# Performance work log

Measured on AMD Instinct MI355X. Metric: run time of the kernel, lower is better.

Reference implementation:

```python
import jax, jax.numpy as jnp
import numpy as np


def _oneplus(x):
    return 1.0 + jax.nn.softplus(x)


def _content(mem, keys, beta):
    # mem: [B,A,M], keys: [B,K,M], beta: [B,K] -> weights [B,K,A]
    eps = 1e-6
    dot = jnp.einsum('bam,bkm->bka', mem, keys)
    mn = jnp.linalg.norm(mem, axis=-1)   # [B,A]
    kn = jnp.linalg.norm(keys, axis=-1)  # [B,K]
    cos = dot / (kn[:, :, None] * mn[:, None, :] + eps)
    return jax.nn.softmax(beta[:, :, None] * cos, axis=-1)


def setup_inputs():
    key = jax.random.key(0)
    ks = jax.random.split(key, 20)
    B, I, H, O, A, M, R = 16, 256, 512, 256, 1024, 64, 4
    IF = R * M + R + M + 1 + M + M + R + 2 + 3 * R  # 471
    def lin(k, fi, fo):
        return jax.random.normal(k, (fi, fo)) / np.sqrt(fi)
    eye = jnp.eye(A)
    return dict(
        x=jax.random.normal(ks[0], (B, I)),
        h_prev=jax.random.normal(ks[1], (B, H)) * 0.1,
        c_prev=jax.random.normal(ks[2], (B, H)) * 0.1,
        mem_prev=jax.random.normal(ks[3], (B, A, M)) * 0.1,
        rw_prev=jax.nn.softmax(jax.random.normal(ks[4], (B, R, A)), axis=-1),
        ww_prev=jax.nn.softmax(jax.random.normal(ks[5], (B, A)), axis=-1),
        usage_prev=jax.random.uniform(ks[6], (B, A)),
        prec_prev=jax.nn.softmax(jax.random.normal(ks[7], (B, A)), axis=-1),
        link_prev=jax.random.uniform(ks[8], (B, A, A)) * 1e-3 * (1.0 - eye),
        rv_prev=jax.random.normal(ks[9], (B, R * M)) * 0.1,
        Wx=lin(ks[10], I + R * M, 4 * H),
        Wh=lin(ks[11], H, 4 * H),
        b_lstm=jnp.zeros((4 * H,)),
        W_hid=lin(ks[12], H, O),
        b_hid=jnp.zeros((O,)),
        W_if=lin(ks[13], H, IF),
        b_if=jnp.zeros((IF,)),
        W_rd=lin(ks[14], R * M, O),
        b_rd=jnp.zeros((O,)),
    )


def reference(x, h_prev, c_prev, mem_prev, rw_prev, ww_prev, usage_prev, prec_prev,
              link_prev, rv_prev, Wx, Wh, b_lstm, W_hid, b_hid, W_if, b_if, W_rd, b_rd):
    B, R, A = rw_prev.shape
    M = mem_prev.shape[-1]
    # --- controller LSTM over [input, prev read vectors] ---
    z = jnp.concatenate([x, rv_prev], axis=-1) @ Wx + h_prev @ Wh + b_lstm
    i, f, g, o = jnp.split(z, 4, axis=-1)
    c = jax.nn.sigmoid(f) * c_prev + jax.nn.sigmoid(i) * jnp.tanh(g)
    h = jax.nn.sigmoid(o) * jnp.tanh(c)
    out_hidden = h @ W_hid + b_hid
    iface = h @ W_if + b_if
    # --- split interface vector ---
    p = 0
    k_r = iface[:, p:p + R * M].reshape(B, R, M); p += R * M
    beta_r = _oneplus(iface[:, p:p + R]); p += R
    k_w = iface[:, p:p + M]; p += M
    beta_w = _oneplus(iface[:, p:p + 1]); p += 1
    erase = jax.nn.sigmoid(iface[:, p:p + M]); p += M
    write_v = iface[:, p:p + M]; p += M
    free = jax.nn.sigmoid(iface[:, p:p + R]); p += R
    g_a = jax.nn.sigmoid(iface[:, p:p + 1]); p += 1
    g_w = jax.nn.sigmoid(iface[:, p:p + 1]); p += 1
    pi = jax.nn.softmax(iface[:, p:p + 3 * R].reshape(B, R, 3), axis=-1)
    # --- usage / retention ---
    psi = jnp.prod(1.0 - free[:, :, None] * rw_prev, axis=1)  # [B,A]
    usage = (usage_prev + ww_prev - usage_prev * ww_prev) * psi
    # --- allocation weighting via sorted usage ---
    idx = jnp.argsort(usage, axis=-1)
    su = jnp.take_along_axis(usage, idx, axis=-1)
    cp = jnp.cumprod(su, axis=-1)
    cp_excl = jnp.concatenate([jnp.ones_like(cp[:, :1]), cp[:, :-1]], axis=-1)
    a_sorted = (1.0 - su) * cp_excl
    alloc = jnp.take_along_axis(a_sorted, jnp.argsort(idx, axis=-1), axis=-1)
    # --- write weighting + memory edit ---
    c_w = _content(mem_prev, k_w[:, None, :], beta_w)[:, 0]  # [B,A]
    ww = g_w * (g_a * alloc + (1.0 - g_a) * c_w)
    mem = mem_prev * (1.0 - ww[:, :, None] * erase[:, None, :]) + ww[:, :, None] * write_v[:, None, :]
    # --- temporal link / precedence ---
    link = (1.0 - ww[:, :, None] - ww[:, None, :]) * link_prev + ww[:, :, None] * prec_prev[:, None, :]
    link = link * (1.0 - jnp.eye(A, dtype=link.dtype))
    prec = (1.0 - jnp.sum(ww, axis=-1, keepdims=True)) * prec_prev + ww
    # --- read weighting: backward / content / forward modes ---
    fwd_w = jnp.einsum('bij,brj->bri', link, rw_prev)
    bwd_w = jnp.einsum('bji,brj->bri', link, rw_prev)
    c_r = _content(mem, k_r, beta_r)
    w_r = pi[..., 0:1] * bwd_w + pi[..., 1:2] * c_r + pi[..., 2:3] * fwd_w
    rv = jnp.einsum('bra,bam->brm', w_r, mem).reshape(B, R * M)
    return out_hidden + rv @ W_rd + b_rd
```

## Files before the change

kernel.cpp:

```cpp
#include <hip/hip_runtime.h>
#include <math.h>


__device__ __forceinline__ float sigf(float x){ return 1.0f/(1.0f+expf(-x)); }
__device__ __forceinline__ float softplusf(float x){ return fmaxf(x,0.0f)+log1pf(expf(-fabsf(x))); }

__global__ __launch_bounds__(256) void k_lstm_part(const float* __restrict__ x,
    const float* __restrict__ rv, const float* __restrict__ hp,
    const float* __restrict__ Wx, const float* __restrict__ Wh,
    float* __restrict__ zpart){
  __shared__ float inp[8][64];
  int ct = blockIdx.x, kt = blockIdx.y, bg = blockIdx.z, t = threadIdx.x;
  for (int i = t; i < 512; i += 256){
    int bb = i >> 6, kk = i & 63;
    int k = kt*64 + kk, b = bg*8 + bb;
    float v = (k < 256) ? x[b*256+k] : (k < 512) ? rv[b*256 + k-256] : hp[b*512 + k-512];
    inp[bb][kk] = v;
  }
  __syncthreads();
  int col = ct*256 + t;
  float acc[8];
  #pragma unroll
  for (int bb = 0; bb < 8; ++bb) acc[bb] = 0.0f;
  for (int kk = 0; kk < 64; ++kk){
    int k = kt*64 + kk;
    float w = (k < 512) ? Wx[(long)k*2048 + col] : Wh[(long)(k-512)*2048 + col];
    #pragma unroll
    for (int bb = 0; bb < 8; ++bb) acc[bb] += inp[bb][kk]*w;
  }
  #pragma unroll
  for (int bb = 0; bb < 8; ++bb)
    zpart[((long)kt*16 + bg*8 + bb)*2048 + col] = acc[bb];
}

__global__ void k_lstm_fin(const float* __restrict__ zpart, const float* __restrict__ bl,
                           const float* __restrict__ cp, float* __restrict__ h_ws){
  int jt = blockIdx.x, b = blockIdx.y, j = jt*128 + threadIdx.x;
  float zi = bl[j], zf = bl[512+j], zg = bl[1024+j], zo = bl[1536+j];
  for (int kt = 0; kt < 16; ++kt){
    const float* zp = zpart + ((long)kt*16 + b)*2048;
    zi += zp[j]; zf += zp[512+j]; zg += zp[1024+j]; zo += zp[1536+j];
  }
  float c = sigf(zf)*cp[b*512+j] + sigf(zi)*tanhf(zg);
  h_ws[b*512+j] = sigf(zo)*tanhf(c);
}

__global__ __launch_bounds__(256) void k_iface_part(const float* __restrict__ h_ws,
    const float* __restrict__ W_if, const float* __restrict__ W_hid,
    float* __restrict__ ifpart){
  __shared__ float hh[8][32];
  int ct = blockIdx.x, kt = blockIdx.y, bg = blockIdx.z, t = threadIdx.x;
  {
    int bb = t >> 5, kk = t & 31;
    hh[bb][kk] = h_ws[(bg*8 + bb)*512 + kt*32 + kk];
  }
  __syncthreads();
  int col = ct*256 + t;
  float acc[8];
  #pragma unroll
  for (int bb = 0; bb < 8; ++bb) acc[bb] = 0.0f;
  if (col < 727){
    for (int kk = 0; kk < 32; ++kk){
      int k = kt*32 + kk;
      float w = (col < 471) ? W_if[(long)k*471 + col] : W_hid[(long)k*256 + (col-471)];
      #pragma unroll
      for (int bb = 0; bb < 8; ++bb) acc[bb] += hh[bb][kk]*w;
    }
    #pragma unroll
    for (int bb = 0; bb < 8; ++bb)
      ifpart[((long)kt*16 + bg*8 + bb)*768 + col] = acc[bb];
  }
}

__global__ void k_iface_fin(const float* __restrict__ ifpart, const float* __restrict__ b_if,
                            const float* __restrict__ b_hid, float* __restrict__ ifr_ws,
                            float* __restrict__ outh_ws){
  int b = blockIdx.x, t = threadIdx.x;
  if (t >= 727) return;
  float s = (t < 471) ? b_if[t] : b_hid[t-471];
  for (int kt = 0; kt < 16; ++kt) s += ifpart[((long)kt*16 + b)*768 + t];
  if (t < 471) ifr_ws[b*512 + t] = s;
  else         outh_ws[b*256 + (t-471)] = s;
}

__global__ void k_act_alloc(const float* __restrict__ ifr_ws, const float* __restrict__ rw_prev,
                            const float* __restrict__ ww_prev, const float* __restrict__ usage_prev,
                            float* __restrict__ ifa_ws, float* __restrict__ alloc_ws){
  __shared__ float sifa[480];
  __shared__ unsigned long long keys[1024];
  __shared__ float cpp[1024];
  int b = blockIdx.x, t = threadIdx.x;
  const float* ifr = ifr_ws + b*512;
  if (t < 471){
    float v = ifr[t], o = v;
    if ((t >= 256 && t < 260) || t == 324) o = 1.0f + softplusf(v);
    else if ((t >= 325 && t < 389) || (t >= 453 && t < 459)) o = sigf(v);
    sifa[t] = o;
  }
  __syncthreads();
  if (t < 4){
    float p0 = ifr[459+t*3+0], p1 = ifr[459+t*3+1], p2 = ifr[459+t*3+2];
    float mx = fmaxf(p0, fmaxf(p1,p2));
    float e0 = expf(p0-mx), e1 = expf(p1-mx), e2 = expf(p2-mx);
    float s = e0+e1+e2;
    sifa[459+t*3+0]=e0/s; sifa[459+t*3+1]=e1/s; sifa[459+t*3+2]=e2/s;
  }
  __syncthreads();
  if (t < 471) ifa_ws[b*512 + t] = sifa[t];
  float f0 = sifa[453], f1 = sifa[454], f2 = sifa[455], f3 = sifa[456];
  float psi = (1.f - f0*rw_prev[(long)(b*4+0)*1024 + t])
            * (1.f - f1*rw_prev[(long)(b*4+1)*1024 + t])
            * (1.f - f2*rw_prev[(long)(b*4+2)*1024 + t])
            * (1.f - f3*rw_prev[(long)(b*4+3)*1024 + t]);
  float uu = usage_prev[b*1024+t], w = ww_prev[b*1024+t];
  float uval = (uu + w - uu*w) * psi;
  unsigned int ub = __float_as_uint(uval);
  unsigned int k32 = ub ^ (((int)ub >> 31) | 0x80000000u);
  keys[t] = ((unsigned long long)k32 << 32) | (unsigned int)t;
  __syncthreads();
  for (int k = 2; k <= 1024; k <<= 1){
    for (int j = k >> 1; j > 0; j >>= 1){
      int ixj = t ^ j;
      if (ixj > t){
        unsigned long long a = keys[t], c = keys[ixj];
        bool up = ((t & k) == 0);
        if ((a > c) == up){ keys[t] = c; keys[ixj] = a; }
      }
      __syncthreads();
    }
  }
  unsigned long long key = keys[t];
  unsigned int hk = (unsigned int)(key >> 32);
  unsigned int ob = (hk & 0x80000000u) ? (hk ^ 0x80000000u) : ~hk;
  float su = __uint_as_float(ob);
  int oi = (int)(key & 1023u);
  cpp[t] = su;
  __syncthreads();
  for (int off = 1; off < 1024; off <<= 1){
    float tmp = (t >= off) ? cpp[t-off] : 1.0f;
    __syncthreads();
    cpp[t] *= tmp;
    __syncthreads();
  }
  float cpe = (t == 0) ? 1.0f : cpp[t-1];
  alloc_ws[b*1024 + oi] = (1.0f - su) * cpe;
}

__global__ __launch_bounds__(256) void k_wscore(const float* __restrict__ mem_prev,
    const float* __restrict__ ifa_ws, float* __restrict__ wsc_ws){
  int at = blockIdx.x, b = blockIdx.y;
  int t = threadIdx.x, w = t >> 6, m = t & 63;
  const float* ifa = ifa_ws + b*512;
  float kwm = ifa[260+m], beta = ifa[324];
  float knsq = kwm*kwm;
  for (int o = 32; o > 0; o >>= 1) knsq += __shfl_xor(knsq, o);
  float kn = sqrtf(knsq);
  for (int rr = 0; rr < 16; ++rr){
    int a = at*64 + w*16 + rr;
    float v = mem_prev[((long)b*1024+a)*64+m];
    float d = v*kwm, sq = v*v;
    for (int o = 32; o > 0; o >>= 1){ d += __shfl_xor(d,o); sq += __shfl_xor(sq,o); }
    if (m == 0) wsc_ws[b*1024+a] = beta*d/(kn*sqrtf(sq)+1e-6f);
  }
}

__global__ void k_cw_ww(const float* __restrict__ wsc_ws, const float* __restrict__ ifa_ws,
                        const float* __restrict__ alloc_ws, const float* __restrict__ rw_prev,
                        float* __restrict__ ww_ws, float* __restrict__ e_ws){
  __shared__ float red[1024];
  int b = blockIdx.x, t = threadIdx.x;
  const float* ifa = ifa_ws + b*512;
  float g_a = ifa[457], g_w = ifa[458];
  float sc = wsc_ws[b*1024+t];
  red[t] = sc; __syncthreads();
  for (int s = 512; s > 0; s >>= 1){ if (t < s) red[t] = fmaxf(red[t], red[t+s]); __syncthreads(); }
  float mx = red[0]; __syncthreads();
  float e = expf(sc - mx);
  red[t] = e; __syncthreads();
  for (int s = 512; s > 0; s >>= 1){ if (t < s) red[t] += red[t+s]; __syncthreads(); }
  float cw = e / red[0];
  float ww = g_w*(g_a*alloc_ws[b*1024+t] + (1.0f-g_a)*cw);
  ww_ws[b*1024+t] = ww;
  #pragma unroll
  for (int r = 0; r < 4; ++r)
    e_ws[(long)(b*4+r)*1024 + t] = ww * rw_prev[(long)(b*4+r)*1024 + t];
}

__global__ __launch_bounds__(256) void k_score(const float* __restrict__ mem_prev,
    const float* __restrict__ ww_ws, const float* __restrict__ ifa_ws,
    float* __restrict__ mnorm_ws, float* __restrict__ rdot_ws){
  int at = blockIdx.x, b = blockIdx.y;
  int t = threadIdx.x, w = t >> 6, m = t & 63;
  const float* ifa = ifa_ws + b*512;
  float er = ifa[325+m], wv = ifa[389+m];
  float k0 = ifa[m], k1 = ifa[64+m], k2 = ifa[128+m], k3 = ifa[192+m];
  for (int rr = 0; rr < 16; ++rr){
    int a = at*64 + w*16 + rr;
    float ww = ww_ws[b*1024+a];
    float v = mem_prev[((long)b*1024+a)*64+m]*(1.0f - ww*er) + ww*wv;
    float sq = v*v, d0 = v*k0, d1 = v*k1, d2 = v*k2, d3 = v*k3;
    for (int o = 32; o > 0; o >>= 1){
      sq += __shfl_xor(sq,o); d0 += __shfl_xor(d0,o); d1 += __shfl_xor(d1,o);
      d2 += __shfl_xor(d2,o); d3 += __shfl_xor(d3,o);
    }
    if (m == 0){
      mnorm_ws[b*1024+a] = sqrtf(sq);
      rdot_ws[(long)(b*4+0)*1024+a] = d0; rdot_ws[(long)(b*4+1)*1024+a] = d1;
      rdot_ws[(long)(b*4+2)*1024+a] = d2; rdot_ws[(long)(b*4+3)*1024+a] = d3;
    }
  }
}

__global__ __launch_bounds__(256) void k_linkfb(const float* __restrict__ link_prev,
    const float* __restrict__ rw_prev, const float* __restrict__ e_ws,
    const float* __restrict__ prec_prev, const float* __restrict__ ww_ws,
    float* __restrict__ fwd_part, float* __restrict__ bwd_part){
  __shared__ float Lt[64][68];
  int band = blockIdx.x, ct = blockIdx.y, b = blockIdx.z, t = threadIdx.x;
  int r = t >> 6, lane = t & 63;
  int ru = __builtin_amdgcn_readfirstlane(r);
  const float4* L4 = (const float4*)link_prev;
  #pragma unroll
  for (int q = 0; q < 4; ++q){
    int idx = t + 256*q;
    int row = idx >> 4, c4 = idx & 15;
    float4 v = L4[((long)b << 18) + (long)(band*64+row)*256 + ct*16 + c4];
    *(float4*)&Lt[row][c4*4] = v;
  }
  const float* aJ = rw_prev + (long)(b*4+ru)*1024 + ct*64;
  const float* eJ = e_ws    + (long)(b*4+ru)*1024 + ct*64;
  const float* aI = rw_prev + (long)(b*4+ru)*1024 + band*64;
  const float* eI = e_ws    + (long)(b*4+ru)*1024 + band*64;
  float pv = prec_prev[b*1024 + ct*64 + lane] * aJ[lane];
  float wvs = eI[lane];
  for (int o = 32; o > 0; o >>= 1){ pv += __shfl_xor(pv,o); wvs += __shfl_xor(wvs,o); }
  float wwi = ww_ws[b*1024 + band*64 + lane];
  float wwc = ww_ws[b*1024 + ct*64 + lane];
  float pc  = prec_prev[b*1024 + ct*64 + lane];
  __syncthreads();
  float A1 = 0.0f, A2 = 0.0f;
  for (int jc = 0; jc < 64; jc += 4){
    float4 Lv = *(const float4*)&Lt[lane][jc];
    A1 += Lv.x*aJ[jc] + Lv.y*aJ[jc+1] + Lv.z*aJ[jc+2] + Lv.w*aJ[jc+3];
    A2 += Lv.x*eJ[jc] + Lv.y*eJ[jc+1] + Lv.z*eJ[jc+2] + Lv.w*eJ[jc+3];
  }
  float facc = (1.0f - wwi)*A1 - A2 + wwi*pv;
  float B1 = 0.0f, B2 = 0.0f;
  for (int rowl = 0; rowl < 64; ++rowl){
    float Lv = Lt[rowl][lane];
    B1 += Lv * aI[rowl];
    B2 += Lv * eI[rowl];
  }
  float bacc = (1.0f - wwc)*B1 - B2 + pc*wvs;
  if (band == ct){
    float D = ((1.0f - 2.0f*wwi)*Lt[lane][lane] + wwi*pc)*aJ[lane];
    facc -= D;
    bacc -= D;
  }
  fwd_part[(long)ct*65536 + (long)(b*4+r)*1024 + band*64 + lane] = facc;
  bwd_part[(long)band*65536 + (long)(b*4+r)*1024 + ct*64 + lane] = bacc;
}

__global__ void k_fbred(const float* __restrict__ fwd_part, const float* __restrict__ bwd_part,
                        float* __restrict__ fwd_ws, float* __restrict__ bwd_ws){
  int idx = blockIdx.x*1024 + threadIdx.x;
  float f = 0.0f, bsum = 0.0f;
  #pragma unroll
  for (int c = 0; c < 16; ++c){
    f    += fwd_part[(long)c*65536 + idx];
    bsum += bwd_part[(long)c*65536 + idx];
  }
  fwd_ws[idx] = f;
  bwd_ws[idx] = bsum;
}

__global__ void k_read(const float* __restrict__ rdot_ws, const float* __restrict__ mnorm_ws,
                       const float* __restrict__ ifa_ws, const float* __restrict__ fwd_ws,
                       const float* __restrict__ bwd_ws, const float* __restrict__ mem_prev,
                       const float* __restrict__ ww_ws, float* __restrict__ rv_ws){
  __shared__ float red[1024]; __shared__ float wrs[1024]; __shared__ float wwsh[1024];
  __shared__ float par[1];
  int r = blockIdx.x, b = blockIdx.y, t = threadIdx.x;
  const float* ifa = ifa_ws + b*512;
  if (t == 0){
    float s = 0;
    for (int m = 0; m < 64; ++m){ float v = ifa[r*64+m]; s += v*v; }
    par[0] = sqrtf(s);
  }
  wwsh[t] = ww_ws[b*1024+t];
  __syncthreads();
  float kn = par[0], beta = ifa[256 + r];
  float sc = beta * rdot_ws[(long)(b*4+r)*1024 + t] / (kn*mnorm_ws[b*1024+t] + 1e-6f);
  red[t] = sc; __syncthreads();
  for (int s = 512; s > 0; s >>= 1){ if (t < s) red[t] = fmaxf(red[t], red[t+s]); __syncthreads(); }
  float mx = red[0]; __syncthreads();
  float e = expf(sc - mx);
  red[t] = e; __syncthreads();
  for (int s = 512; s > 0; s >>= 1){ if (t < s) red[t] += red[t+s]; __syncthreads(); }
  float cr = e / red[0];
  __syncthreads();
  float p0 = ifa[459+3*r], p1 = ifa[460+3*r], p2 = ifa[461+3*r];
  wrs[t] = p0*bwd_ws[(long)(b*4+r)*1024 + t] + p1*cr + p2*fwd_ws[(long)(b*4+r)*1024 + t];
  __syncthreads();
  int m = t & 63, ch = t >> 6;
  float er = ifa[325+m], wv = ifa[389+m];
  float acc = 0;
  for (int q = 0; q < 64; ++q){
    int a = ch*64 + q;
    float w = wwsh[a];
    float v = mem_prev[((long)b*1024 + a)*64 + m]*(1.0f - w*er) + w*wv;
    acc += wrs[a]*v;
  }
  red[ch*64 + m] = acc;
  __syncthreads();
  if (t < 64){
    float s = 0;
    for (int c2 = 0; c2 < 16; ++c2) s += red[c2*64 + t];
    rv_ws[(b*4+r)*64 + t] = s;
  }
}

__global__ void k_out(const float* __restrict__ outh_ws, const float* __restrict__ rv_ws,
                      const float* __restrict__ W_rd, const float* __restrict__ b_rd,
                      float* __restrict__ out){
  __shared__ float rvs[256]; __shared__ float part[4][256];
  int b = blockIdx.x, t = threadIdx.x;
  int o = t & 255, kq = t >> 8;
  if (t < 256) rvs[t] = rv_ws[b*256 + t];
  __syncthreads();
  float acc = 0.0f;
  for (int q = kq*64; q < kq*64 + 64; ++q) acc += rvs[q]*W_rd[(long)q*256 + o];
  part[kq][o] = acc;
  __syncthreads();
  if (t < 256)
    out[b*256+t] = outh_ws[b*256+t] + b_rd[t] + part[0][t] + part[1][t] + part[2][t] + part[3][t];
}

extern "C" void kernel_launch(void* const* d_in, const int* in_sizes, int n_in,
                              void* d_out, int out_size, void* d_ws, size_t ws_size,
                              hipStream_t stream){
  const float* x          = (const float*)d_in[0];
  const float* h_prev     = (const float*)d_in[1];
  const float* c_prev     = (const float*)d_in[2];
  const float* mem_prev   = (const float*)d_in[3];
  const float* rw_prev    = (const float*)d_in[4];
  const float* ww_prev    = (const float*)d_in[5];
  const float* usage_prev = (const float*)d_in[6];
  const float* prec_prev  = (const float*)d_in[7];
  const float* link_prev  = (const float*)d_in[8];
  const float* rv_prev    = (const float*)d_in[9];
  const float* Wx         = (const float*)d_in[10];
  const float* Wh         = (const float*)d_in[11];
  const float* b_lstm     = (const float*)d_in[12];
  const float* W_hid      = (const float*)d_in[13];
  const float* b_hid      = (const float*)d_in[14];
  const float* W_if       = (const float*)d_in[15];
  const float* b_if       = (const float*)d_in[16];
  const float* W_rd       = (const float*)d_in[17];
  const float* b_rd       = (const float*)d_in[18];
  float* out = (float*)d_out;

  float* ws = (float*)d_ws;
  float* h_ws     = ws + 0;
  float* ifr_ws   = ws + 8192;
  float* ifa_ws   = ws + 16384;
  float* outh_ws  = ws + 24576;
  float* alloc_ws = ws + 28672;
  float* ww_ws    = ws + 45056;
  float* mnorm_ws = ws + 61440;
  float* wsc_ws   = ws + 77824;
  float* rv_ws    = ws + 94208;
  float* fwd_ws   = ws + 98304;
  float* bwd_ws   = ws + 163840;
  float* rdot_ws  = ws + 229376;
  float* e_ws     = ws + 294912;
  float* zpart    = ws + 360448;
  float* ifpart   = ws + 884736;
  float* fwd_part = ws + 1081344;
  float* bwd_part = ws + 2129920;

  k_lstm_part<<<dim3(8,16,2),256,0,stream>>>(x, rv_prev, h_prev, Wx, Wh, zpart);
  k_lstm_fin<<<dim3(4,16),128,0,stream>>>(zpart, b_lstm, c_prev, h_ws);
  k_iface_part<<<dim3(3,16,2),256,0,stream>>>(h_ws, W_if, W_hid, ifpart);
  k_iface_fin<<<16,768,0,stream>>>(ifpart, b_if, b_hid, ifr_ws, outh_ws);
  k_act_alloc<<<16,1024,0,stream>>>(ifr_ws, rw_prev, ww_prev, usage_prev, ifa_ws, alloc_ws);
  k_wscore<<<dim3(16,16),256,0,stream>>>(mem_prev, ifa_ws, wsc_ws);
  k_cw_ww<<<16,1024,0,stream>>>(wsc_ws, ifa_ws, alloc_ws, rw_prev, ww_ws, e_ws);
  k_score<<<dim3(16,16),256,0,stream>>>(mem_prev, ww_ws, ifa_ws, mnorm_ws, rdot_ws);
  k_linkfb<<<dim3(16,16,16),256,0,stream>>>(link_prev, rw_prev, e_ws, prec_prev, ww_ws,
                                            fwd_part, bwd_part);
  k_fbred<<<64,1024,0,stream>>>(fwd_part, bwd_part, fwd_ws, bwd_ws);
  k_read<<<dim3(4,16),1024,0,stream>>>(rdot_ws, mnorm_ws, ifa_ws, fwd_ws, bwd_ws,
                                       mem_prev, ww_ws, rv_ws);
  k_out<<<16,1024,0,stream>>>(outh_ws, rv_ws, W_rd, b_rd, out);
}
```

Baseline: 240.2 us.

## Use wave shuffles for sort, scan and softmax; fuse partial reduction into read

Bitonic sort stages with stride under 64 now exchange keys through wavefront shuffles instead of shared memory and barriers. The cumulative-product scan becomes a per-wave shuffle scan followed by a cross-wave prefix, and the softmax reductions in the write and read kernels become wave reductions plus a 16-entry combine. The separate forward/backward partial-sum kernel is removed and its 16-way sum folded into the read kernel, saving a launch and a round trip through global memory. The score kernels also move to 512-thread blocks with fewer rows per wave, which changes the per-thread work split.

```diff
diff --git a/kernel.cpp b/kernel.cpp
--- a/kernel.cpp
+++ b/kernel.cpp
@@ -88,8 +88,9 @@
                             float* __restrict__ ifa_ws, float* __restrict__ alloc_ws){
   __shared__ float sifa[480];
   __shared__ unsigned long long keys[1024];
-  __shared__ float cpp[1024];
+  __shared__ float wtot[16];
   int b = blockIdx.x, t = threadIdx.x;
+  int lane = t & 63, wid = t >> 6;
   const float* ifr = ifr_ws + b*512;
   if (t < 471){
     float v = ifr[t], o = v;
@@ -116,37 +117,44 @@
   float uval = (uu + w - uu*w) * psi;
   unsigned int ub = __float_as_uint(uval);
   unsigned int k32 = ub ^ (((int)ub >> 31) | 0x80000000u);
-  keys[t] = ((unsigned long long)k32 << 32) | (unsigned int)t;
-  __syncthreads();
-  for (int k = 2; k <= 1024; k <<= 1){
-    for (int j = k >> 1; j > 0; j >>= 1){
-      int ixj = t ^ j;
-      if (ixj > t){
-        unsigned long long a = keys[t], c = keys[ixj];
-        bool up = ((t & k) == 0);
-        if ((a > c) == up){ keys[t] = c; keys[ixj] = a; }
+  unsigned long long key = ((unsigned long long)k32 << 32) | (unsigned int)t;
+  for (int kk2 = 2; kk2 <= 1024; kk2 <<= 1){
+    for (int j = kk2 >> 1; j > 0; j >>= 1){
+      unsigned long long other;
+      if (j >= 64){
+        keys[t] = key;
+        __syncthreads();
+        other = keys[t ^ j];
+        __syncthreads();
+      } else {
+        other = __shfl_xor(key, j);
       }
-      __syncthreads();
+      bool up = ((t & kk2) == 0);
+      bool keepMin = (((t & j) == 0) == up);
+      if (keepMin ? (other < key) : (other > key)) key = other;
     }
   }
-  unsigned long long key = keys[t];
   unsigned int hk = (unsigned int)(key >> 32);
   unsigned int ob = (hk & 0x80000000u) ? (hk ^ 0x80000000u) : ~hk;
   float su = __uint_as_float(ob);
   int oi = (int)(key & 1023u);
-  cpp[t] = su;
-  __syncthreads();
-  for (int off = 1; off < 1024; off <<= 1){
-    float tmp = (t >= off) ? cpp[t-off] : 1.0f;
-    __syncthreads();
-    cpp[t] *= tmp;
-    __syncthreads();
-  }
-  float cpe = (t == 0) ? 1.0f : cpp[t-1];
+  float s = su;
+  #pragma unroll
+  for (int off = 1; off < 64; off <<= 1){
+    float v = __shfl_up(s, off);
+    if (lane >= off) s *= v;
+  }
+  if (lane == 63) wtot[wid] = s;
+  __syncthreads();
+  float wpre = 1.0f;
+  for (int w2 = 0; w2 < wid; ++w2) wpre *= wtot[w2];
+  float ex = __shfl_up(s, 1);
+  if (lane == 0) ex = 1.0f;
+  float cpe = ex * wpre;
   alloc_ws[b*1024 + oi] = (1.0f - su) * cpe;
 }
 
-__global__ __launch_bounds__(256) void k_wscore(const float* __restrict__ mem_prev,
+__global__ __launch_bounds__(512) void k_wscore(const float* __restrict__ mem_prev,
     const float* __restrict__ ifa_ws, float* __restrict__ wsc_ws){
   int at = blockIdx.x, b = blockIdx.y;
   int t = threadIdx.x, w = t >> 6, m = t & 63;
@@ -155,8 +163,8 @@
   float knsq = kwm*kwm;
   for (int o = 32; o > 0; o >>= 1) knsq += __shfl_xor(knsq, o);
   float kn = sqrtf(knsq);
-  for (int rr = 0; rr < 16; ++rr){
-    int a = at*64 + w*16 + rr;
+  for (int rr = 0; rr < 8; ++rr){
+    int a = at*64 + w*8 + rr;
     float v = mem_prev[((long)b*1024+a)*64+m];
     float d = v*kwm, sq = v*v;
     for (int o = 32; o > 0; o >>= 1){ d += __shfl_xor(d,o); sq += __shfl_xor(sq,o); }
@@ -167,18 +175,27 @@
 __global__ void k_cw_ww(const float* __restrict__ wsc_ws, const float* __restrict__ ifa_ws,
                         const float* __restrict__ alloc_ws, const float* __restrict__ rw_prev,
                         float* __restrict__ ww_ws, float* __restrict__ e_ws){
-  __shared__ float red[1024];
-  int b = blockIdx.x, t = threadIdx.x;
+  __shared__ float wred[16]; __shared__ float wred2[16];
+  int b = blockIdx.x, t = threadIdx.x, lane = t & 63, wid = t >> 6;
   const float* ifa = ifa_ws + b*512;
   float g_a = ifa[457], g_w = ifa[458];
   float sc = wsc_ws[b*1024+t];
-  red[t] = sc; __syncthreads();
-  for (int s = 512; s > 0; s >>= 1){ if (t < s) red[t] = fmaxf(red[t], red[t+s]); __syncthreads(); }
-  float mx = red[0]; __syncthreads();
+  float m = sc;
+  for (int o = 32; o > 0; o >>= 1) m = fmaxf(m, __shfl_xor(m, o));
+  if (lane == 0) wred[wid] = m;
+  __syncthreads();
+  float mx = wred[0];
+  #pragma unroll
+  for (int i = 1; i < 16; ++i) mx = fmaxf(mx, wred[i]);
   float e = expf(sc - mx);
-  red[t] = e; __syncthreads();
-  for (int s = 512; s > 0; s >>= 1){ if (t < s) red[t] += red[t+s]; __syncthreads(); }
-  float cw = e / red[0];
+  float ssum = e;
+  for (int o = 32; o > 0; o >>= 1) ssum += __shfl_xor(ssum, o);
+  if (lane == 0) wred2[wid] = ssum;
+  __syncthreads();
+  float tot = 0.0f;
+  #pragma unroll
+  for (int i = 0; i < 16; ++i) tot += wred2[i];
+  float cw = e / tot;
   float ww = g_w*(g_a*alloc_ws[b*1024+t] + (1.0f-g_a)*cw);
   ww_ws[b*1024+t] = ww;
   #pragma unroll
@@ -186,7 +203,7 @@
     e_ws[(long)(b*4+r)*1024 + t] = ww * rw_prev[(long)(b*4+r)*1024 + t];
 }
 
-__global__ __launch_bounds__(256) void k_score(const float* __restrict__ mem_prev,
+__global__ __launch_bounds__(512) void k_score(const float* __restrict__ mem_prev,
     const float* __restrict__ ww_ws, const float* __restrict__ ifa_ws,
     float* __restrict__ mnorm_ws, float* __restrict__ rdot_ws){
   int at = blockIdx.x, b = blockIdx.y;
@@ -194,8 +211,8 @@
   const float* ifa = ifa_ws + b*512;
   float er = ifa[325+m], wv = ifa[389+m];
   float k0 = ifa[m], k1 = ifa[64+m], k2 = ifa[128+m], k3 = ifa[192+m];
-  for (int rr = 0; rr < 16; ++rr){
-    int a = at*64 + w*16 + rr;
+  for (int rr = 0; rr < 8; ++rr){
+    int a = at*64 + w*8 + rr;
     float ww = ww_ws[b*1024+a];
     float v = mem_prev[((long)b*1024+a)*64+m]*(1.0f - ww*er) + ww*wv;
     float sq = v*v, d0 = v*k0, d1 = v*k1, d2 = v*k2, d3 = v*k3;
@@ -261,62 +278,66 @@
   bwd_part[(long)band*65536 + (long)(b*4+r)*1024 + ct*64 + lane] = bacc;
 }
 
-__global__ void k_fbred(const float* __restrict__ fwd_part, const float* __restrict__ bwd_part,
-                        float* __restrict__ fwd_ws, float* __restrict__ bwd_ws){
-  int idx = blockIdx.x*1024 + threadIdx.x;
-  float f = 0.0f, bsum = 0.0f;
-  #pragma unroll
-  for (int c = 0; c < 16; ++c){
-    f    += fwd_part[(long)c*65536 + idx];
-    bsum += bwd_part[(long)c*65536 + idx];
-  }
-  fwd_ws[idx] = f;
-  bwd_ws[idx] = bsum;
-}
-
 __global__ void k_read(const float* __restrict__ rdot_ws, const float* __restrict__ mnorm_ws,
-                       const float* __restrict__ ifa_ws, const float* __restrict__ fwd_ws,
-                       const float* __restrict__ bwd_ws, const float* __restrict__ mem_prev,
+                       const float* __restrict__ ifa_ws, const float* __restrict__ fwd_part,
+                       const float* __restrict__ bwd_part, const float* __restrict__ mem_prev,
                        const float* __restrict__ ww_ws, float* __restrict__ rv_ws){
   __shared__ float red[1024]; __shared__ float wrs[1024]; __shared__ float wwsh[1024];
-  __shared__ float par[1];
+  __shared__ float par[1]; __shared__ float wred[16]; __shared__ float wred2[16];
   int r = blockIdx.x, b = blockIdx.y, t = threadIdx.x;
+  int lane = t & 63, wid = t >> 6;
   const float* ifa = ifa_ws + b*512;
-  if (t == 0){
-    float s = 0;
-    for (int m = 0; m < 64; ++m){ float v = ifa[r*64+m]; s += v*v; }
-    par[0] = sqrtf(s);
+  long base = (long)(b*4+r)*1024 + t;
+  float fsum = 0.0f, bsum = 0.0f;
+  #pragma unroll
+  for (int c = 0; c < 16; ++c){
+    fsum += fwd_part[(long)c*65536 + base];
+    bsum += bwd_part[(long)c*65536 + base];
+  }
+  if (t < 64){
+    float v = ifa[r*64+t];
+    float sq = v*v;
+    for (int o = 32; o > 0; o >>= 1) sq += __shfl_xor(sq, o);
+    if (t == 0) par[0] = sqrtf(sq);
   }
   wwsh[t] = ww_ws[b*1024+t];
   __syncthreads();
   float kn = par[0], beta = ifa[256 + r];
-  float sc = beta * rdot_ws[(long)(b*4+r)*1024 + t] / (kn*mnorm_ws[b*1024+t] + 1e-6f);
-  red[t] = sc; __syncthreads();
-  for (int s = 512; s > 0; s >>= 1){ if (t < s) red[t] = fmaxf(red[t], red[t+s]); __syncthreads(); }
-  float mx = red[0]; __syncthreads();
+  float sc = beta * rdot_ws[base] / (kn*mnorm_ws[b*1024+t] + 1e-6f);
+  float m = sc;
+  for (int o = 32; o > 0; o >>= 1) m = fmaxf(m, __shfl_xor(m, o));
+  if (lane == 0) wred[wid] = m;
+  __syncthreads();
+  float mx = wred[0];
+  #pragma unroll
+  for (int i = 1; i < 16; ++i) mx = fmaxf(mx, wred[i]);
   float e = expf(sc - mx);
-  red[t] = e; __syncthreads();
-  for (int s = 512; s > 0; s >>= 1){ if (t < s) red[t] += red[t+s]; __syncthreads(); }
-  float cr = e / red[0];
-  __syncthreads();
+  float s = e;
+  for (int o = 32; o > 0; o >>= 1) s += __shfl_xor(s, o);
+  if (lane == 0) wred2[wid] = s;
+  __syncthreads();
+  float tot = 0.0f;
+  #pragma unroll
+  for (int i = 0; i < 16; ++i) tot += wred2[i];
+  float cr = e / tot;
   float p0 = ifa[459+3*r], p1 = ifa[460+3*r], p2 = ifa[461+3*r];
-  wrs[t] = p0*bwd_ws[(long)(b*4+r)*1024 + t] + p1*cr + p2*fwd_ws[(long)(b*4+r)*1024 + t];
-  __syncthreads();
-  int m = t & 63, ch = t >> 6;
-  float er = ifa[325+m], wv = ifa[389+m];
+  wrs[t] = p0*bsum + p1*cr + p2*fsum;
+  __syncthreads();
+  int mm = t & 63, ch = t >> 6;
+  float er = ifa[325+mm], wv = ifa[389+mm];
   float acc = 0;
   for (int q = 0; q < 64; ++q){
     int a = ch*64 + q;
     float w = wwsh[a];
-    float v = mem_prev[((long)b*1024 + a)*64 + m]*(1.0f - w*er) + w*wv;
+    float v = mem_prev[((long)b*1024 + a)*64 + mm]*(1.0f - w*er) + w*wv;
     acc += wrs[a]*v;
   }
-  red[ch*64 + m] = acc;
+  red[ch*64 + mm] = acc;
   __syncthreads();
   if (t < 64){
-    float s = 0;
-    for (int c2 = 0; c2 < 16; ++c2) s += red[c2*64 + t];
-    rv_ws[(b*4+r)*64 + t] = s;
+    float s2 = 0;
+    for (int c2 = 0; c2 < 16; ++c2) s2 += red[c2*64 + t];
+    rv_ws[(b*4+r)*64 + t] = s2;
   }
 }
 
@@ -378,19 +399,19 @@
   float* ifpart   = ws + 884736;
   float* fwd_part = ws + 1081344;
   float* bwd_part = ws + 2129920;
+  (void)fwd_ws; (void)bwd_ws;
 
   k_lstm_part<<<dim3(8,16,2),256,0,stream>>>(x, rv_prev, h_prev, Wx, Wh, zpart);
   k_lstm_fin<<<dim3(4,16),128,0,stream>>>(zpart, b_lstm, c_prev, h_ws);
   k_iface_part<<<dim3(3,16,2),256,0,stream>>>(h_ws, W_if, W_hid, ifpart);
   k_iface_fin<<<16,768,0,stream>>>(ifpart, b_if, b_hid, ifr_ws, outh_ws);
   k_act_alloc<<<16,1024,0,stream>>>(ifr_ws, rw_prev, ww_prev, usage_prev, ifa_ws, alloc_ws);
-  k_wscore<<<dim3(16,16),256,0,stream>>>(mem_prev, ifa_ws, wsc_ws);
+  k_wscore<<<dim3(16,16),512,0,stream>>>(mem_prev, ifa_ws, wsc_ws);
   k_cw_ww<<<16,1024,0,stream>>>(wsc_ws, ifa_ws, alloc_ws, rw_prev, ww_ws, e_ws);
-  k_score<<<dim3(16,16),256,0,stream>>>(mem_prev, ww_ws, ifa_ws, mnorm_ws, rdot_ws);
+  k_score<<<dim3(16,16),512,0,stream>>>(mem_prev, ww_ws, ifa_ws, mnorm_ws, rdot_ws);
   k_linkfb<<<dim3(16,16,16),256,0,stream>>>(link_prev, rw_prev, e_ws, prec_prev, ww_ws,
                                             fwd_part, bwd_part);
-  k_fbred<<<64,1024,0,stream>>>(fwd_part, bwd_part, fwd_ws, bwd_ws);
-  k_read<<<dim3(4,16),1024,0,stream>>>(rdot_ws, mnorm_ws, ifa_ws, fwd_ws, bwd_ws,
+  k_read<<<dim3(4,16),1024,0,stream>>>(rdot_ws, mnorm_ws, ifa_ws, fwd_part, bwd_part,
                                        mem_prev, ww_ws, rv_ws);
   k_out<<<16,1024,0,stream>>>(outh_ws, rv_ws, W_rd, b_rd, out);
 }
```

Measured after the change: 229.5 us. -4.5%, faster.
